# Optimization experiments

Measured on AMD Instinct MI355X. Metric: run time of the kernel, lower is better.

## Reference

```python
import jax, jax.numpy as jnp
import numpy as np
from jax import lax

N, CIN, COUT = 10000, 64, 32
RADIUS = 0.07
K = 32            # cap on neighbors per query (radius search truncated to K nearest)
KSIZE = 3         # kernel_size = [3,3,3]
NCELLS = KSIZE ** 3

# 8 trilinear corner offsets
_OFFS = np.array([[i, j, k] for i in (0, 1) for j in (0, 1) for k in (0, 1)], dtype=np.int32)  # (8,3)
_STRIDE = np.array([KSIZE * KSIZE, KSIZE, 1], dtype=np.int32)


def setup_inputs() -> dict:
    key = jax.random.key(0)
    k1, k2, k3 = jax.random.split(key, 3)
    points = jax.random.uniform(k1, (N, 3), dtype=jnp.float32)
    feats = jax.random.normal(k2, (N, CIN), dtype=jnp.float32)
    # ContinuousConv kernel: [3,3,3,Cin,Cout] flattened to [27,Cin,Cout]
    W = jax.random.normal(k3, (NCELLS, CIN, COUT), dtype=jnp.float32) * 0.05
    b = jnp.zeros((COUT,), dtype=jnp.float32)
    return {"feats": feats, "points": points, "W": W, "b": b}


def _neighbors(points):
    # squared pairwise distances (N,N); radius search truncated to K nearest
    sq = jnp.sum(points * points, axis=-1)
    d2 = sq[:, None] + sq[None, :] - 2.0 * (points @ points.T)
    neg_d2, idx = lax.top_k(-d2, K)           # (N,K)
    valid = (-neg_d2) <= RADIUS * RADIUS      # (N,K) bool
    return idx, valid


def _cconv(feats, points, W, b, idx, valid):
    nb_pos = points[idx]                      # (N,K,3) gather
    rel = (nb_pos - points[:, None, :]) / RADIUS   # normalized by half-extent -> unit ball
    # ball_to_cube_radial: v -> v * ||v||_2 / ||v||_inf  (0 at origin)
    l2 = jnp.linalg.norm(rel, axis=-1, keepdims=True)
    linf = jnp.max(jnp.abs(rel), axis=-1, keepdims=True)
    t = jnp.where(linf > 0, rel * (l2 / jnp.maximum(linf, 1e-12)), 0.0)  # in [-1,1]^3
    # map to kernel grid coords in [0, KSIZE-1]
    coords = (t + 1.0) * 0.5 * (KSIZE - 1)    # (N,K,3)
    c0 = jnp.clip(jnp.floor(coords), 0, KSIZE - 2)
    f = coords - c0                            # trilinear fractions, (N,K,3)
    offs = jnp.asarray(_OFFS)                  # (8,3)
    # trilinear weights (N,K,8)
    fw = jnp.where(offs[None, None] == 1, f[:, :, None, :], 1.0 - f[:, :, None, :])
    w8 = jnp.prod(fw, axis=-1)
    # flattened corner cell indices (N,K,8)
    cidx = jnp.sum((c0[:, :, None, :].astype(jnp.int32) + offs) * jnp.asarray(_STRIDE), axis=-1)
    onehot = jax.nn.one_hot(cidx, NCELLS, dtype=feats.dtype)        # (N,K,8,27)
    wmass = jnp.einsum('nke,nkej->nkj', w8, onehot)                 # (N,K,27)
    wmass = wmass * valid[:, :, None].astype(feats.dtype)
    nb_feats = feats[idx]                                           # (N,K,Cin)
    A = jnp.einsum('nkj,nkf->njf', wmass, nb_feats)                 # (N,27,Cin)
    out = jnp.einsum('njf,jfo->no', A, W)                           # (N,Cout)
    # normalize=True: divide by neighbor importance sum (count, window=None)
    nn = jnp.sum(valid.astype(feats.dtype), axis=-1)
    out = out / jnp.maximum(nn, 1.0)[:, None] + b
    return out


@jax.jit
def reference(feats, points, W, b):
    idx, valid = _neighbors(points)
    return _cconv(feats, points, W, b, idx, valid)
```

## Files before the change

### kernel.cpp

```cpp
#include <hip/hip_runtime.h>
#include <math.h>

#define N_PTS   10000
#define CIN     64
#define COUT    32
#define KCAP    32
#define RADIUSF 0.07f
#define NCELLS  27
#define QB      8
#define MAXC    48
#define GRES    14
#define GCELLS  (GRES * GRES * GRES)
#define CPAD    72
#define NSCAT   40
#define WT_ELEMS (NCELLS * COUT * CIN)

typedef __attribute__((ext_vector_type(8))) short         bf16x8_t;
typedef __attribute__((ext_vector_type(4))) float         f32x4_t;

__device__ __forceinline__ void cell_coords(float x, float y, float z,
                                            int& cx, int& cy, int& cz) {
    cx = (int)(x * (float)GRES); if (cx > GRES - 1) cx = GRES - 1; if (cx < 0) cx = 0;
    cy = (int)(y * (float)GRES); if (cy > GRES - 1) cy = GRES - 1; if (cy < 0) cy = 0;
    cz = (int)(z * (float)GRES); if (cz > GRES - 1) cz = GRES - 1; if (cz < 0) cz = 0;
}

__device__ __forceinline__ unsigned int f2bf_u(float x) {
    unsigned int u = __float_as_uint(x);
    return (u + 0x7FFFu + ((u >> 16) & 1u)) >> 16;
}

__global__ __launch_bounds__(1024) void k1_hist_scan_wt(
    const float* __restrict__ pts,
    const float* __restrict__ W,
    int* __restrict__ offsets,
    int* __restrict__ cursor,
    unsigned short* __restrict__ Wt)
{
    const int t = threadIdx.x;
    const int b = blockIdx.x;

    if (b >= 1) {
        __shared__ float tile[CIN * 33];
        const int cell = b - 1;
        for (int idx = t; idx < CIN * COUT; idx += 1024) {
            int f = idx >> 5, o = idx & 31;
            tile[f * 33 + o] = W[cell * (CIN * COUT) + idx];
        }
        __syncthreads();
        for (int idx = t; idx < CIN * COUT; idx += 1024) {
            int o = idx >> 6, f = idx & 63;
            Wt[cell * (CIN * COUT) + idx] = (unsigned short)f2bf_u(tile[f * 33 + o]);
        }
        return;
    }

    __shared__ int s_hist[GCELLS];
    __shared__ int s_wsum[16];
    const int lane = t & 63;
    const int wv   = t >> 6;

    for (int i = t; i < GCELLS; i += 1024) s_hist[i] = 0;
    __syncthreads();
    for (int i = t; i < N_PTS; i += 1024) {
        int cx, cy, cz;
        cell_coords(pts[3 * i], pts[3 * i + 1], pts[3 * i + 2], cx, cy, cz);
        atomicAdd(&s_hist[(cx * GRES + cy) * GRES + cz], 1);
    }
    __syncthreads();

    const int c0 = t * 3;
    int v0 = (c0 + 0 < GCELLS) ? s_hist[c0 + 0] : 0;
    int v1 = (c0 + 1 < GCELLS) ? s_hist[c0 + 1] : 0;
    int v2 = (c0 + 2 < GCELLS) ? s_hist[c0 + 2] : 0;
    const int local = v0 + v1 + v2;
    int inc = local;
    #pragma unroll
    for (int d = 1; d < 64; d <<= 1) {
        int up = __shfl_up(inc, d);
        if (lane >= d) inc += up;
    }
    if (lane == 63) s_wsum[wv] = inc;
    __syncthreads();
    if (t == 0) {
        int run = 0;
        #pragma unroll
        for (int i = 0; i < 16; ++i) { int tmp = s_wsum[i]; s_wsum[i] = run; run += tmp; }
    }
    __syncthreads();
    int base = s_wsum[wv] + (inc - local);
    if (c0 + 0 < GCELLS) { offsets[c0 + 0] = base; cursor[c0 + 0] = base; base += v0; }
    if (c0 + 1 < GCELLS) { offsets[c0 + 1] = base; cursor[c0 + 1] = base; base += v1; }
    if (c0 + 2 < GCELLS) { offsets[c0 + 2] = base; cursor[c0 + 2] = base; base += v2; }
    if (t == 0) offsets[GCELLS] = N_PTS;
}

__global__ __launch_bounds__(256) void k2_scatter(
    const float* __restrict__ pts,
    int*   __restrict__ cursor,
    int*   __restrict__ sorted,
    float* __restrict__ pts_s)
{
    const int b = blockIdx.x;
    const int t = threadIdx.x;
    const int per = N_PTS / NSCAT;
    const int lo = b * per;
    const int hi = lo + per;
    for (int i = lo + t; i < hi; i += 256) {
        float x = pts[3 * i + 0], y = pts[3 * i + 1], z = pts[3 * i + 2];
        int cx, cy, cz;
        cell_coords(x, y, z, cx, cy, cz);
        int cell = (cx * GRES + cy) * GRES + cz;
        int pos = atomicAdd(&cursor[cell], 1);
        sorted[pos] = i;
        pts_s[3 * pos + 0] = x;
        pts_s[3 * pos + 1] = y;
        pts_s[3 * pos + 2] = z;
    }
}

__global__ __launch_bounds__(512) void cconv_grid_mfma_kernel(
    const float* __restrict__ feats,
    const unsigned short* __restrict__ Wt,
    const float* __restrict__ bias,
    const int*   __restrict__ offsets,
    const int*   __restrict__ sorted,
    const float* __restrict__ pts_s,
    float* __restrict__ out)
{
    const int tid  = threadIdx.x;
    const int lane = tid & 63;
    const int wave = tid >> 6;

    __shared__ __align__(16) unsigned short sAb[QB][NCELLS + 1][CPAD];
    __shared__ __align__(16) float s_scratch[2048];
    __shared__ int   s_idx[QB][MAXC];
    __shared__ int   s_org[QB][MAXC];
    __shared__ int   s_sel[QB][KCAP];
    __shared__ int   s_cnt[QB];
    __shared__ int   s_qi[QB];
    __shared__ int   s_nn[QB];

    float (*s_pool)[4][MAXC] = (float (*)[4][MAXC])s_scratch;

    if (lane == 0) s_cnt[wave] = 0;

    const int q_flat = blockIdx.x * QB + wave;
    const int qi = sorted[q_flat];
    const float qx = pts_s[3 * q_flat + 0];
    const float qy = pts_s[3 * q_flat + 1];
    const float qz = pts_s[3 * q_flat + 2];
    const float sqn = qx * qx + qy * qy + qz * qz;
    const float r2 = RADIUSF * RADIUSF;

    int cx, cy, cz;
    cell_coords(qx, qy, qz, cx, cy, cz);

    int zlo = cz - 1; if (zlo < 0) zlo = 0;
    int zhi = cz + 1; if (zhi > GRES - 1) zhi = GRES - 1;
    int ss[9], sl[9];
    #pragma unroll
    for (int dxi = 0; dxi < 3; ++dxi) {
        #pragma unroll
        for (int dyi = 0; dyi < 3; ++dyi) {
            const int ii = dxi * 3 + dyi;
            int cxx = cx + dxi - 1, cyy = cy + dyi - 1;
            bool ok = (cxx >= 0) && (cxx <= GRES - 1) && (cyy >= 0) && (cyy <= GRES - 1);
            int row = ((ok ? cxx : 0) * GRES + (ok ? cyy : 0)) * GRES;
            int s = offsets[row + zlo];
            int e = offsets[row + zhi + 1];
            ss[ii] = s;
            sl[ii] = ok ? (e - s) : 0;
        }
    }
    int cum[10];
    cum[0] = 0;
    #pragma unroll
    for (int ii = 0; ii < 9; ++ii) cum[ii + 1] = cum[ii] + sl[ii];
    const int T = cum[9];

    for (int t = lane; t < T; t += 64) {
        int gidx = 0;
        #pragma unroll
        for (int ii = 0; ii < 9; ++ii) {
            bool in = (t >= cum[ii]) && (t < cum[ii + 1]);
            int cand = ss[ii] + (t - cum[ii]);
            gidx = in ? cand : gidx;
        }
        float x = pts_s[3 * gidx + 0];
        float y = pts_s[3 * gidx + 1];
        float z = pts_s[3 * gidx + 2];
        float sqj = x * x + y * y + z * z;
        float dot = qx * x + qy * y + qz * z;
        float d2 = (sqn + sqj) - 2.0f * dot;
        if (d2 <= r2) {
            int pos = atomicAdd(&s_cnt[wave], 1);
            if (pos < MAXC) {
                s_pool[wave][0][pos] = d2;
                s_pool[wave][1][pos] = x;
                s_pool[wave][2][pos] = y;
                s_pool[wave][3][pos] = z;
                s_idx[wave][pos] = gidx;
            }
        }
    }

    int M = s_cnt[wave]; if (M > MAXC) M = MAXC;
    const int cnt = (M > KCAP) ? KCAP : M;
    const bool over = (M > KCAP);

    if (lane < M) s_org[wave][lane] = sorted[s_idx[wave][lane]];

    if (over) {
        if (lane < M) {
            float dc = s_pool[wave][0][lane];
            int   ic = s_org[wave][lane];
            int rank = 0;
            for (int m = 0; m < M; ++m) {
                float dm = s_pool[wave][0][m];
                int   im = s_org[wave][m];
                rank += (dm < dc || (dm == dc && im < ic)) ? 1 : 0;
            }
            if (rank < KCAP) s_sel[wave][rank] = lane;
        }
    }
    if (lane == 0) { s_qi[wave] = qi; s_nn[wave] = cnt; }

    float* w9w = (float*)&sAb[wave][0][0];
    if (lane < cnt) {
        int slot = over ? s_sel[wave][lane] : lane;
        float x = s_pool[wave][1][slot];
        float y = s_pool[wave][2][slot];
        float z = s_pool[wave][3][slot];
        int   j = s_org[wave][slot];
        float rx = (x - qx) / RADIUSF;
        float ry = (y - qy) / RADIUSF;
        float rz = (z - qz) / RADIUSF;
        float l2 = sqrtf(rx * rx + ry * ry + rz * rz);
        float ax = fabsf(rx), ay = fabsf(ry), az = fabsf(rz);
        float linf = fmaxf(fmaxf(ax, ay), az);
        float s = (linf > 0.0f) ? (l2 / fmaxf(linf, 1e-12f)) : 0.0f;
        float tx = rx * s, ty = ry * s, tz = rz * s;
        float cxf = (tx + 1.0f) * 0.5f * 2.0f;
        float cyf = (ty + 1.0f) * 0.5f * 2.0f;
        float czf = (tz + 1.0f) * 0.5f * 2.0f;
        float c0x = fminf(fmaxf(floorf(cxf), 0.0f), 1.0f);
        float c0y = fminf(fmaxf(floorf(cyf), 0.0f), 1.0f);
        float c0z = fminf(fmaxf(floorf(czf), 0.0f), 1.0f);
        float fx = cxf - c0x;
        float fy = cyf - c0y;
        float fz = czf - c0z;
        int i0 = (int)c0x, i1 = (int)c0y, i2 = (int)c0z;
        float gx0 = 1.0f - fx, gx1 = fx;
        float gy0 = 1.0f - fy, gy1 = fy;
        float gz0 = 1.0f - fz, gz1 = fz;
        float* wp = w9w + lane * 12;
        wp[0] = i0 ? 0.0f : gx0;  wp[1] = i0 ? gx0 : gx1;  wp[2] = i0 ? gx1 : 0.0f;
        wp[3] = i1 ? 0.0f : gy0;  wp[4] = i1 ? gy0 : gy1;  wp[5] = i1 ? gy1 : 0.0f;
        wp[6] = i2 ? 0.0f : gz0;  wp[7] = i2 ? gz0 : gz1;  wp[8] = i2 ? gz1 : 0.0f;
        wp[9] = __int_as_float(j * CIN);
    }

    float a[NCELLS];
    #pragma unroll
    for (int c = 0; c < NCELLS; ++c) a[c] = 0.0f;

    if (cnt > 0) {
        float fvA = feats[__float_as_int(w9w[9]) + lane];
        float fvB = 0.0f;
        if (cnt > 1) fvB = feats[__float_as_int(w9w[12 + 9]) + lane];
        for (int k = 0; k < cnt; ++k) {
            const float* wp = w9w + k * 12;
            float wxv[3] = {wp[0], wp[1], wp[2]};
            float wyv[3] = {wp[3], wp[4], wp[5]};
            float wz0 = wp[6], wz1 = wp[7], wz2 = wp[8];
            float fv_cur = fvA;
            fvA = fvB;
            if (k + 2 < cnt) fvB = feats[__float_as_int(w9w[(k + 2) * 12 + 9]) + lane];
            float pzv[3] = {wz0 * fv_cur, wz1 * fv_cur, wz2 * fv_cur};
            #pragma unroll
            for (int ci = 0; ci < 3; ++ci) {
                #pragma unroll
                for (int cj = 0; cj < 3; ++cj) {
                    float wxy = wxv[ci] * wyv[cj];
                    #pragma unroll
                    for (int ck = 0; ck < 3; ++ck) {
                        a[ci * 9 + cj * 3 + ck] = fmaf(wxy, pzv[ck], a[ci * 9 + cj * 3 + ck]);
                    }
                }
            }
        }
    }
    #pragma unroll
    for (int c = 0; c < NCELLS; ++c) sAb[wave][c][lane] = (unsigned short)f2bf_u(a[c]);
    sAb[wave][NCELLS][lane] = 0;
    __syncthreads();

    f32x4_t acc0 = {0.f, 0.f, 0.f, 0.f};
    f32x4_t acc1 = {0.f, 0.f, 0.f, 0.f};
    const int r  = lane & 15;
    const int kg = lane >> 4;

    #define STEP_ADDR(it, cvar, fvar, cwvar)                                   \
        const int s5_##it = wave + (it) * 8;                                   \
        const int cvar = s5_##it >> 1;                                         \
        const int fvar = (s5_##it & 1) << 5;                                   \
        const int cwvar = (cvar < NCELLS) ? cvar : 0;

    STEP_ADDR(0, c_0, f_0, cw_0)
    bf16x8_t aCur = {}, bCur0, bCur1;
    if (r < QB) aCur = *(const bf16x8_t*)&sAb[r][c_0][f_0 + kg * 8];
    bCur0 = *(const bf16x8_t*)(Wt + ((cw_0 * COUT + r     ) * CIN + f_0 + kg * 8));
    bCur1 = *(const bf16x8_t*)(Wt + ((cw_0 * COUT + 16 + r) * CIN + f_0 + kg * 8));

    #pragma unroll
    for (int it = 0; it < 7; ++it) {
        bf16x8_t aNxt = {}, bNxt0 = {}, bNxt1 = {};
        if (it + 1 < 7) {
            const int s5n = wave + (it + 1) * 8;
            const int cn  = s5n >> 1;
            const int fn  = (s5n & 1) << 5;
            const int cwn = (cn < NCELLS) ? cn : 0;
            if (r < QB) aNxt = *(const bf16x8_t*)&sAb[r][cn][fn + kg * 8];
            bNxt0 = *(const bf16x8_t*)(Wt + ((cwn * COUT + r     ) * CIN + fn + kg * 8));
            bNxt1 = *(const bf16x8_t*)(Wt + ((cwn * COUT + 16 + r) * CIN + fn + kg * 8));
        }
        acc0 = __builtin_amdgcn_mfma_f32_16x16x32_bf16(aCur, bCur0, acc0, 0, 0, 0);
        acc1 = __builtin_amdgcn_mfma_f32_16x16x32_bf16(aCur, bCur1, acc1, 0, 0, 0);
        aCur = aNxt; bCur0 = bNxt0; bCur1 = bNxt1;
    }
    #undef STEP_ADDR

    float (*sC)[QB][COUT] = (float (*)[QB][COUT])s_scratch;
    if (lane < 32) {
        int qrow = (lane >> 4) * 4;
        int o = lane & 15;
        #pragma unroll
        for (int j = 0; j < 4; ++j) {
            sC[wave][qrow + j][o]      = acc0[j];
            sC[wave][qrow + j][16 + o] = acc1[j];
        }
    }
    __syncthreads();

    if (tid < QB * COUT) {
        int q = tid >> 5, o = tid & 31;
        float v = 0.0f;
        #pragma unroll
        for (int w = 0; w < QB; ++w) v += sC[w][q][o];
        float nn = (float)s_nn[q];
        out[s_qi[q] * COUT + o] = v / fmaxf(nn, 1.0f) + bias[o];
    }
}

__global__ __launch_bounds__(64) void cconv_fused_kernel(
    const float* __restrict__ feats,
    const float* __restrict__ points,
    const float* __restrict__ W,
    const float* __restrict__ bias,
    float* __restrict__ out)
{
    const int n    = blockIdx.x;
    const int lane = threadIdx.x;

    __shared__ float sA[NCELLS][CIN];
    __shared__ float s_d2[128];
    __shared__ int   s_idx[128];
    __shared__ int   s_rank[128];
    __shared__ int   s_sel[KCAP];
    __shared__ int   s_cnt;

    if (lane == 0) s_cnt = 0;
    for (int c = lane; c < NCELLS * CIN; c += 64) ((float*)sA)[c] = 0.0f;
    __syncthreads();

    const float qx = points[3 * n + 0];
    const float qy = points[3 * n + 1];
    const float qz = points[3 * n + 2];
    const float sqn = qx * qx + qy * qy + qz * qz;
    const float r2 = RADIUSF * RADIUSF;

    for (int j = lane; j < N_PTS; j += 64) {
        float x = points[3 * j + 0];
        float y = points[3 * j + 1];
        float z = points[3 * j + 2];
        float sqj = x * x + y * y + z * z;
        float dot = qx * x + qy * y + qz * z;
        float d2 = (sqn + sqj) - 2.0f * dot;
        if (d2 <= r2) {
            int pos = atomicAdd(&s_cnt, 1);
            if (pos < 128) { s_d2[pos] = d2; s_idx[pos] = j; }
        }
    }
    __syncthreads();

    int M = s_cnt; if (M > 128) M = 128;
    int cnt;
    if (M > KCAP) {
        for (int c = lane; c < M; c += 64) {
            float dc = s_d2[c]; int ic = s_idx[c]; int rank = 0;
            for (int m = 0; m < M; ++m) {
                float dm = s_d2[m]; int im = s_idx[m];
                rank += (dm < dc || (dm == dc && im < ic)) ? 1 : 0;
            }
            s_rank[c] = rank;
        }
        __syncthreads();
        for (int c = lane; c < M; c += 64) {
            int r = s_rank[c];
            if (r < KCAP) s_sel[r] = s_idx[c];
        }
        __syncthreads();
        cnt = KCAP;
    } else cnt = M;
    const int* nbr = (M > KCAP) ? s_sel : s_idx;

    for (int k = 0; k < cnt; ++k) {
        int j = nbr[k];
        float x = points[3 * j + 0];
        float y = points[3 * j + 1];
        float z = points[3 * j + 2];
        float rx = (x - qx) / RADIUSF;
        float ry = (y - qy) / RADIUSF;
        float rz = (z - qz) / RADIUSF;
        float l2 = sqrtf(rx * rx + ry * ry + rz * rz);
        float ax = fabsf(rx), ay = fabsf(ry), az = fabsf(rz);
        float linf = fmaxf(fmaxf(ax, ay), az);
        float s = (linf > 0.0f) ? (l2 / fmaxf(linf, 1e-12f)) : 0.0f;
        float tx = rx * s, ty = ry * s, tz = rz * s;
        float cxf = (tx + 1.0f) * 0.5f * 2.0f;
        float cyf = (ty + 1.0f) * 0.5f * 2.0f;
        float czf = (tz + 1.0f) * 0.5f * 2.0f;
        float c0x = fminf(fmaxf(floorf(cxf), 0.0f), 1.0f);
        float c0y = fminf(fmaxf(floorf(cyf), 0.0f), 1.0f);
        float c0z = fminf(fmaxf(floorf(czf), 0.0f), 1.0f);
        float fx = cxf - c0x, fy = cyf - c0y, fz = czf - c0z;
        int i0 = (int)c0x, i1 = (int)c0y, i2 = (int)c0z;
        int base = i0 * 9 + i1 * 3 + i2;
        float gx0 = 1.0f - fx, gx1 = fx;
        float gy0 = 1.0f - fy, gy1 = fy;
        float gz0 = 1.0f - fz, gz1 = fz;
        float featv = feats[j * CIN + lane];
        sA[base + 0 ][lane] += (gx0 * gy0) * gz0 * featv;
        sA[base + 1 ][lane] += (gx0 * gy0) * gz1 * featv;
        sA[base + 3 ][lane] += (gx0 * gy1) * gz0 * featv;
        sA[base + 4 ][lane] += (gx0 * gy1) * gz1 * featv;
        sA[base + 9 ][lane] += (gx1 * gy0) * gz0 * featv;
        sA[base + 10][lane] += (gx1 * gy0) * gz1 * featv;
        sA[base + 12][lane] += (gx1 * gy1) * gz0 * featv;
        sA[base + 13][lane] += (gx1 * gy1) * gz1 * featv;
    }
    __syncthreads();

    const int o    = lane & 31;
    const int half = lane >> 5;
    const int c_begin = half ? 14 : 0;
    const int c_end   = half ? 27 : 14;
    float acc = 0.0f;
    for (int cell = c_begin; cell < c_end; ++cell) {
        const float* __restrict__ Wrow = W + (cell * CIN) * COUT + o;
        #pragma unroll 8
        for (int f = 0; f < CIN; ++f) acc += sA[cell][f] * Wrow[f * COUT];
    }
    acc += __shfl_xor(acc, 32);
    if (lane < COUT) {
        float nn = (float)cnt;
        out[n * COUT + lane] = acc / fmaxf(nn, 1.0f) + bias[lane];
    }
}

extern "C" void kernel_launch(void* const* d_in, const int* in_sizes, int n_in,
                              void* d_out, int out_size, void* d_ws, size_t ws_size,
                              hipStream_t stream) {
    const float* feats  = (const float*)d_in[0];
    const float* points = (const float*)d_in[1];
    const float* W      = (const float*)d_in[2];
    const float* bias   = (const float*)d_in[3];
    float* out = (float*)d_out;

    const size_t wt_bytes = (size_t)WT_ELEMS * sizeof(unsigned short);
    const size_t need     = wt_bytes
                          + (size_t)(GCELLS + 1 + GCELLS + N_PTS) * sizeof(int)
                          + (size_t)3 * N_PTS * sizeof(float);

    if (ws_size >= need) {
        unsigned short* Wt = (unsigned short*)d_ws;
        int* offsets = (int*)((char*)d_ws + wt_bytes);
        int* cursor  = offsets + GCELLS + 1;
        int* sorted  = cursor + GCELLS;
        float* pts_s = (float*)(sorted + N_PTS);

        k1_hist_scan_wt<<<1 + NCELLS, 1024, 0, stream>>>(points, W, offsets, cursor, Wt);
        k2_scatter<<<NSCAT, 256, 0, stream>>>(points, cursor, sorted, pts_s);
        cconv_grid_mfma_kernel<<<N_PTS / QB, QB * 64, 0, stream>>>(
            feats, Wt, bias, offsets, sorted, pts_s, out);
    } else {
        cconv_fused_kernel<<<N_PTS, 64, 0, stream>>>(feats, points, W, bias, out);
    }
}
```

Baseline: 105.7 us.

## Alias per-wave scratch into sAb and reduce wave partials with LDS atomics

Moves the per-wave neighbor index, origin and selection arrays into unused space inside each wave's sAb slice, and shrinks the shared scratch buffer. The goal is a smaller LDS footprint per block, which may let more blocks run per CU. The per-wave MFMA partial results are now summed into one shared tile with LDS float atomics instead of eight copies followed by a serial sum; this adds an extra barrier to zero that tile. It also simplifies the candidate-index selection in the grid gather and loads the trilinear weights as 4-wide vectors.

```diff
diff --git a/kernel.cpp b/kernel.cpp
--- a/kernel.cpp
+++ b/kernel.cpp
@@ -133,15 +133,18 @@
     const int wave = tid >> 6;
 
     __shared__ __align__(16) unsigned short sAb[QB][NCELLS + 1][CPAD];
-    __shared__ __align__(16) float s_scratch[2048];
-    __shared__ int   s_idx[QB][MAXC];
-    __shared__ int   s_org[QB][MAXC];
-    __shared__ int   s_sel[QB][KCAP];
+    __shared__ __align__(16) float s_scratch[QB * 4 * MAXC];
     __shared__ int   s_cnt[QB];
     __shared__ int   s_qi[QB];
     __shared__ int   s_nn[QB];
 
     float (*s_pool)[4][MAXC] = (float (*)[4][MAXC])s_scratch;
+
+    char*  wbase = (char*)&sAb[wave][0][0];
+    float* w9w   = (float*)wbase;
+    int*   s_idxw = (int*)(wbase + 1536);
+    int*   s_orgw = (int*)(wbase + 1728);
+    int*   s_selw = (int*)(wbase + 1920);
 
     if (lane == 0) s_cnt[wave] = 0;
 
@@ -158,7 +161,8 @@
 
     int zlo = cz - 1; if (zlo < 0) zlo = 0;
     int zhi = cz + 1; if (zhi > GRES - 1) zhi = GRES - 1;
-    int ss[9], sl[9];
+    int adj[9], cum[10];
+    cum[0] = 0;
     #pragma unroll
     for (int dxi = 0; dxi < 3; ++dxi) {
         #pragma unroll
@@ -169,24 +173,18 @@
             int row = ((ok ? cxx : 0) * GRES + (ok ? cyy : 0)) * GRES;
             int s = offsets[row + zlo];
             int e = offsets[row + zhi + 1];
-            ss[ii] = s;
-            sl[ii] = ok ? (e - s) : 0;
-        }
-    }
-    int cum[10];
-    cum[0] = 0;
-    #pragma unroll
-    for (int ii = 0; ii < 9; ++ii) cum[ii + 1] = cum[ii] + sl[ii];
+            int len = ok ? (e - s) : 0;
+            adj[ii] = s - cum[ii];
+            cum[ii + 1] = cum[ii] + len;
+        }
+    }
     const int T = cum[9];
 
     for (int t = lane; t < T; t += 64) {
-        int gidx = 0;
+        int a = adj[0];
         #pragma unroll
-        for (int ii = 0; ii < 9; ++ii) {
-            bool in = (t >= cum[ii]) && (t < cum[ii + 1]);
-            int cand = ss[ii] + (t - cum[ii]);
-            gidx = in ? cand : gidx;
-        }
+        for (int ii = 1; ii < 9; ++ii) a = (t >= cum[ii]) ? adj[ii] : a;
+        const int gidx = a + t;
         float x = pts_s[3 * gidx + 0];
         float y = pts_s[3 * gidx + 1];
         float z = pts_s[3 * gidx + 2];
@@ -200,7 +198,7 @@
                 s_pool[wave][1][pos] = x;
                 s_pool[wave][2][pos] = y;
                 s_pool[wave][3][pos] = z;
-                s_idx[wave][pos] = gidx;
+                s_idxw[pos] = gidx;
             }
         }
     }
@@ -209,30 +207,29 @@
     const int cnt = (M > KCAP) ? KCAP : M;
     const bool over = (M > KCAP);
 
-    if (lane < M) s_org[wave][lane] = sorted[s_idx[wave][lane]];
+    if (lane < M) s_orgw[lane] = sorted[s_idxw[lane]];
 
     if (over) {
         if (lane < M) {
             float dc = s_pool[wave][0][lane];
-            int   ic = s_org[wave][lane];
+            int   ic = s_orgw[lane];
             int rank = 0;
             for (int m = 0; m < M; ++m) {
                 float dm = s_pool[wave][0][m];
-                int   im = s_org[wave][m];
+                int   im = s_orgw[m];
                 rank += (dm < dc || (dm == dc && im < ic)) ? 1 : 0;
             }
-            if (rank < KCAP) s_sel[wave][rank] = lane;
+            if (rank < KCAP) s_selw[rank] = lane;
         }
     }
     if (lane == 0) { s_qi[wave] = qi; s_nn[wave] = cnt; }
 
-    float* w9w = (float*)&sAb[wave][0][0];
     if (lane < cnt) {
-        int slot = over ? s_sel[wave][lane] : lane;
+        int slot = over ? s_selw[lane] : lane;
         float x = s_pool[wave][1][slot];
         float y = s_pool[wave][2][slot];
         float z = s_pool[wave][3][slot];
-        int   j = s_org[wave][slot];
+        int   j = s_orgw[slot];
         float rx = (x - qx) / RADIUSF;
         float ry = (y - qy) / RADIUSF;
         float rz = (z - qz) / RADIUSF;
@@ -255,10 +252,11 @@
         float gy0 = 1.0f - fy, gy1 = fy;
         float gz0 = 1.0f - fz, gz1 = fz;
         float* wp = w9w + lane * 12;
-        wp[0] = i0 ? 0.0f : gx0;  wp[1] = i0 ? gx0 : gx1;  wp[2] = i0 ? gx1 : 0.0f;
-        wp[3] = i1 ? 0.0f : gy0;  wp[4] = i1 ? gy0 : gy1;  wp[5] = i1 ? gy1 : 0.0f;
-        wp[6] = i2 ? 0.0f : gz0;  wp[7] = i2 ? gz0 : gz1;  wp[8] = i2 ? gz1 : 0.0f;
+        wp[0] = i0 ? 0.0f : gx0;  wp[1] = i0 ? gx0 : gx1;  wp[2]  = i0 ? gx1 : 0.0f;
+        wp[3] = i1 ? 0.0f : gy0;  wp[4] = i1 ? gy0 : gy1;  wp[5]  = i1 ? gy1 : 0.0f;
+        wp[6] = i2 ? 0.0f : gz0;  wp[7] = i2 ? gz0 : gz1;  wp[8]  = i2 ? gz1 : 0.0f;
         wp[9] = __int_as_float(j * CIN);
+        wp[10] = 0.0f; wp[11] = 0.0f;
     }
 
     float a[NCELLS];
@@ -271,13 +269,15 @@
         if (cnt > 1) fvB = feats[__float_as_int(w9w[12 + 9]) + lane];
         for (int k = 0; k < cnt; ++k) {
             const float* wp = w9w + k * 12;
-            float wxv[3] = {wp[0], wp[1], wp[2]};
-            float wyv[3] = {wp[3], wp[4], wp[5]};
-            float wz0 = wp[6], wz1 = wp[7], wz2 = wp[8];
+            f32x4_t wv0 = *(const f32x4_t*)(wp);
+            f32x4_t wv1 = *(const f32x4_t*)(wp + 4);
+            float   wz2 = wp[8];
+            float wxv[3] = {wv0[0], wv0[1], wv0[2]};
+            float wyv[3] = {wv0[3], wv1[0], wv1[1]};
             float fv_cur = fvA;
             fvA = fvB;
             if (k + 2 < cnt) fvB = feats[__float_as_int(w9w[(k + 2) * 12 + 9]) + lane];
-            float pzv[3] = {wz0 * fv_cur, wz1 * fv_cur, wz2 * fv_cur};
+            float pzv[3] = {wv1[2] * fv_cur, wv1[3] * fv_cur, wz2 * fv_cur};
             #pragma unroll
             for (int ci = 0; ci < 3; ++ci) {
                 #pragma unroll
@@ -296,22 +296,21 @@
     sAb[wave][NCELLS][lane] = 0;
     __syncthreads();
 
+    if (tid < 256) s_scratch[tid] = 0.0f;
+    __syncthreads();
+
     f32x4_t acc0 = {0.f, 0.f, 0.f, 0.f};
     f32x4_t acc1 = {0.f, 0.f, 0.f, 0.f};
     const int r  = lane & 15;
     const int kg = lane >> 4;
 
-    #define STEP_ADDR(it, cvar, fvar, cwvar)                                   \
-        const int s5_##it = wave + (it) * 8;                                   \
-        const int cvar = s5_##it >> 1;                                         \
-        const int fvar = (s5_##it & 1) << 5;                                   \
-        const int cwvar = (cvar < NCELLS) ? cvar : 0;
-
-    STEP_ADDR(0, c_0, f_0, cw_0)
+    const int s5_0 = wave;
+    const int c_0  = s5_0 >> 1;
+    const int f_0  = (s5_0 & 1) << 5;
     bf16x8_t aCur = {}, bCur0, bCur1;
     if (r < QB) aCur = *(const bf16x8_t*)&sAb[r][c_0][f_0 + kg * 8];
-    bCur0 = *(const bf16x8_t*)(Wt + ((cw_0 * COUT + r     ) * CIN + f_0 + kg * 8));
-    bCur1 = *(const bf16x8_t*)(Wt + ((cw_0 * COUT + 16 + r) * CIN + f_0 + kg * 8));
+    bCur0 = *(const bf16x8_t*)(Wt + ((c_0 * COUT + r     ) * CIN + f_0 + kg * 8));
+    bCur1 = *(const bf16x8_t*)(Wt + ((c_0 * COUT + 16 + r) * CIN + f_0 + kg * 8));
 
     #pragma unroll
     for (int it = 0; it < 7; ++it) {
@@ -329,27 +328,23 @@
         acc1 = __builtin_amdgcn_mfma_f32_16x16x32_bf16(aCur, bCur1, acc1, 0, 0, 0);
         aCur = aNxt; bCur0 = bNxt0; bCur1 = bNxt1;
     }
-    #undef STEP_ADDR
-
-    float (*sC)[QB][COUT] = (float (*)[QB][COUT])s_scratch;
+
+    float (*sC)[COUT] = (float (*)[COUT])s_scratch;
     if (lane < 32) {
         int qrow = (lane >> 4) * 4;
         int o = lane & 15;
         #pragma unroll
         for (int j = 0; j < 4; ++j) {
-            sC[wave][qrow + j][o]      = acc0[j];
-            sC[wave][qrow + j][16 + o] = acc1[j];
+            atomicAdd(&sC[qrow + j][o],      acc0[j]);
+            atomicAdd(&sC[qrow + j][16 + o], acc1[j]);
         }
     }
     __syncthreads();
 
     if (tid < QB * COUT) {
         int q = tid >> 5, o = tid & 31;
-        float v = 0.0f;
-        #pragma unroll
-        for (int w = 0; w < QB; ++w) v += sC[w][q][o];
         float nn = (float)s_nn[q];
-        out[s_qi[q] * COUT + o] = v / fmaxf(nn, 1.0f) + bias[o];
+        out[s_qi[q] * COUT + o] = sC[q][o] / fmaxf(nn, 1.0f) + bias[o];
     }
 }
 
```

New measurement: 114.4 us. 1.08x slower.
